# Kernel optimization log

Hardware: AMD Instinct MI355X
Metric: run time of the kernel (lower is better)

The kernel has to match this reference:

```python
import jax, jax.numpy as jnp
import numpy as np

B, DIN, N = 8, 256, 2048  # batch, input_dim (orig node_num), attention nodes (orig seq_len)


def setup_inputs() -> dict:
    key = jax.random.key(0)
    k1, k2, k3, k4 = jax.random.split(key, 4)
    x = jax.random.normal(k1, (B, DIN, N), jnp.float32)
    adj = jax.random.randint(k2, (N, N), 0, 2).astype(jnp.int32)  # binary adjacency
    W = jax.random.normal(k3, (DIN, DIN), jnp.float32) * 0.05      # Linear(D, D, bias=False), stored (out, in)
    a = jax.random.normal(k4, (3 * DIN,), jnp.float32) * 0.05      # Linear(3D, 1, bias=False)
    return {"x": x, "adj": adj, "W": W, "a": a}


def reference(x, adj, W, a):
    # x: (B, D, N) -> permute to (B, N, D); attention is over the N axis
    xt = jnp.transpose(x, (0, 2, 1))
    h = xt @ W.T                                   # (B, N, D)
    sim = jnp.einsum('bid,bjd->bij', h, h)         # (B, N, N) pairwise dot products
    n = adj.shape[0]
    # neighbor mask: adj nonzero, diagonal forced off (mask[:, i] = 0 in the loop)
    m = (adj != 0) & (~jnp.eye(n, dtype=bool))
    # context: the torch loop's weighted_h is independent of its k axis, so
    # context[b, k, i, d] == C[b, i, d] = sum_j m[i,j] * sim[b,i,j] * h[b,j,d]
    C = jnp.einsum('bij,bjd->bid', jnp.where(m[None, :, :], sim, 0.0), h)  # (B, N, D)
    d = h.shape[-1]
    a1, a2, a3 = a[:d], a[d:2 * d], a[2 * d:]
    # a([h_i, h_j, C_j]) = a1.h_i + a2.h_j + a3.C_j  (concat never materialized)
    s_i = h @ a1                                   # (B, N)
    s_j = h @ a2 + C @ a3                          # (B, N)
    scores = jax.nn.leaky_relu(s_i[:, :, None] + s_j[:, None, :], negative_slope=0.2)
    scores = jnp.where(adj[None, :, :] == 0, jnp.float32(-9e15), scores)
    return jax.nn.softmax(scores, axis=-1)         # (B, N, N)
```

## Files before the change

kernel.cpp:

```cpp
#include <hip/hip_runtime.h>
#include <hip/hip_bf16.h>
#include <math.h>

#define Bq   8
#define DINq 256
#define Nq   2048

typedef __attribute__((ext_vector_type(8))) short bf16x8v;
typedef __attribute__((ext_vector_type(4))) float f32x4v;

__device__ __forceinline__ unsigned short f2bf(float f) {
  union { float f; unsigned u; } v; v.f = f;
  unsigned r = v.u + 0x7fffu + ((v.u >> 16) & 1u);
  return (unsigned short)(r >> 16);
}
__device__ __forceinline__ float bf2f(unsigned short h) {
  union { unsigned u; float f; } v; v.u = ((unsigned)h) << 16;
  return v.f;
}

__device__ __forceinline__ void gld_lds16(const void* g, void* l) {
  __builtin_amdgcn_global_load_lds(
      (const __attribute__((address_space(1))) unsigned int*)g,
      (__attribute__((address_space(3))) unsigned int*)l, 16, 0, 0);
}

__global__ void k_prep(const float* __restrict__ W, const float* __restrict__ a,
                       float* __restrict__ w123) {
  int k = threadIdx.x;
  float s1 = 0.f, s2 = 0.f, s3 = 0.f;
  for (int d = 0; d < DINq; ++d) {
    float w = W[d * DINq + k];
    s1 += w * a[d];
    s2 += w * a[DINq + d];
    s3 += w * a[2 * DINq + d];
  }
  w123[k] = s1; w123[DINq + k] = s2; w123[2 * DINq + k] = s3;
}

__global__ void k_transposeW(const float* __restrict__ W, float* __restrict__ WT) {
  int d = blockIdx.x, k = threadIdx.x;
  WT[(size_t)k * DINq + d] = W[(size_t)d * DINq + k];
}

__global__ void k_tsisb(const float* __restrict__ x, const float* __restrict__ w123,
                        float* __restrict__ tA, float* __restrict__ siA,
                        float* __restrict__ sbA) {
  int b = blockIdx.y;
  int il = threadIdx.x & 63;
  int i = blockIdx.x * 64 + il;
  int ks = (threadIdx.x >> 6) * 64;
  float a1 = 0.f, a2 = 0.f, a3 = 0.f;
  for (int k = ks; k < ks + 64; ++k) {
    float xv = x[((size_t)b * DINq + k) * Nq + i];
    a1 += xv * w123[k];
    a2 += xv * w123[DINq + k];
    a3 += xv * w123[2 * DINq + k];
  }
  __shared__ float r1[256], r2[256], r3[256];
  r1[threadIdx.x] = a1; r2[threadIdx.x] = a2; r3[threadIdx.x] = a3;
  __syncthreads();
  if (threadIdx.x < 64) {
    int l = threadIdx.x;
    float v1 = r1[l] + r1[64 + l] + r1[128 + l] + r1[192 + l];
    float v2 = r2[l] + r2[64 + l] + r2[128 + l] + r2[192 + l];
    float v3 = r3[l] + r3[64 + l] + r3[128 + l] + r3[192 + l];
    int ii = blockIdx.x * 64 + l;
    siA[(size_t)b * Nq + ii] = v1;
    sbA[(size_t)b * Nq + ii] = v2;
    tA[(size_t)b * Nq + ii] = v3;
  }
}

__global__ void k_hX(const float* __restrict__ x, const float* __restrict__ WT,
                     const float* __restrict__ tA, float* __restrict__ h,
                     unsigned short* __restrict__ Xhi, unsigned short* __restrict__ Xlo) {
  __shared__ float xs[64][64];
  __shared__ float ws[64][128];
  const int tid = threadIdx.x;
  const int iq = tid & 15;
  const int dg = tid >> 4;
  const int i0 = blockIdx.x * 64;
  const int dh = blockIdx.y;
  const int b = blockIdx.z;

  float acc[4][8];
#pragma unroll
  for (int aa = 0; aa < 4; ++aa)
#pragma unroll
    for (int cc = 0; cc < 8; ++cc) acc[aa][cc] = 0.f;

  for (int kc = 0; kc < 4; ++kc) {
#pragma unroll
    for (int n = 0; n < 16; ++n) {
      int idx = n * 256 + tid;
      int kk = idx >> 6, ii = idx & 63;
      xs[kk][ii] = x[((size_t)b * DINq + kc * 64 + kk) * Nq + i0 + ii];
    }
#pragma unroll
    for (int n = 0; n < 8; ++n) {
      int idx = n * 256 + tid;
      int kk = idx >> 5, c4 = (idx & 31) * 4;
      *(f32x4v*)&ws[kk][c4] =
          *(const f32x4v*)&WT[(size_t)(kc * 64 + kk) * DINq + dh * 128 + c4];
    }
    __syncthreads();
#pragma unroll 4
    for (int kk = 0; kk < 64; ++kk) {
      f32x4v xv = *(const f32x4v*)&xs[kk][iq * 4];
      f32x4v w0 = *(const f32x4v*)&ws[kk][dg * 8];
      f32x4v w1 = *(const f32x4v*)&ws[kk][dg * 8 + 4];
#pragma unroll
      for (int aa = 0; aa < 4; ++aa) {
#pragma unroll
        for (int cc = 0; cc < 4; ++cc) {
          acc[aa][cc]     += xv[aa] * w0[cc];
          acc[aa][cc + 4] += xv[aa] * w1[cc];
        }
      }
    }
    __syncthreads();
  }

  const int ib = i0 + iq * 4;
  float tv[4];
#pragma unroll
  for (int aa = 0; aa < 4; ++aa) tv[aa] = tA[(size_t)b * Nq + ib + aa];

#pragma unroll
  for (int aa = 0; aa < 4; ++aa) {
    size_t hoff = ((size_t)b * Nq + ib + aa) * DINq + dh * 128 + dg * 8;
    f32x4v h0, h1;
#pragma unroll
    for (int cc = 0; cc < 4; ++cc) { h0[cc] = acc[aa][cc]; h1[cc] = acc[aa][cc + 4]; }
    *(f32x4v*)&h[hoff] = h0;
    *(f32x4v*)&h[hoff + 4] = h1;
  }
#pragma unroll
  for (int cc = 0; cc < 8; ++cc) {
    int d = dh * 128 + dg * 8 + cc;
    unsigned short hv[4], lv[4];
#pragma unroll
    for (int aa = 0; aa < 4; ++aa) {
      float Xv = tv[aa] * acc[aa][cc];
      unsigned short hs = f2bf(Xv);
      hv[aa] = hs;
      lv[aa] = f2bf(Xv - bf2f(hs));
    }
    size_t xoff = ((size_t)b * DINq + d) * Nq + ib;
    *(ushort4*)&Xhi[xoff] = make_ushort4(hv[0], hv[1], hv[2], hv[3]);
    *(ushort4*)&Xlo[xoff] = make_ushort4(lv[0], lv[1], lv[2], lv[3]);
  }
}

__global__ void k_mask(const int* __restrict__ adj, unsigned short* __restrict__ Mb) {
  size_t idx = ((size_t)blockIdx.x * 256 + threadIdx.x) * 8;
  int i = (int)(idx >> 11);
  int j0 = (int)(idx & (Nq - 1));
  const int4* ap = (const int4*)&adj[idx];
  int4 a0 = ap[0], a1 = ap[1];
  int av[8] = {a0.x, a0.y, a0.z, a0.w, a1.x, a1.y, a1.z, a1.w};
  unsigned short v[8];
#pragma unroll
  for (int q = 0; q < 8; ++q)
    v[q] = (av[q] != 0 && (j0 + q) != i) ? (unsigned short)0x3F80 : (unsigned short)0;
  ushort4* mp = (ushort4*)&Mb[idx];
  mp[0] = make_ushort4(v[0], v[1], v[2], v[3]);
  mp[1] = make_ushort4(v[4], v[5], v[6], v[7]);
}

__global__ __launch_bounds__(256, 2) void k_gemm(const unsigned short* __restrict__ Mb,
                                                 const unsigned short* __restrict__ Xhi,
                                                 const unsigned short* __restrict__ Xlo,
                                                 const float* __restrict__ h,
                                                 float* __restrict__ sjp) {
  __shared__ __align__(16) unsigned short As[3][128 * 32];
  __shared__ __align__(16) unsigned short Bs[3][128 * 32];
  const int tid = threadIdx.x;
  const int lane = tid & 63;
  const int wave = tid >> 6;
  const int wr = wave >> 1, wc = wave & 1;
  const int i0 = blockIdx.y * 128, c0 = blockIdx.x * 128;
  const int z = blockIdx.z;
  const unsigned short* __restrict__ Xp = z ? Xlo : Xhi;
  const int r15 = lane & 15, kg = lane >> 4;
  const int kb = (kg * 16) ^ ((r15 & 3) << 4);

  f32x4v acc[4][4];
#pragma unroll
  for (int m = 0; m < 4; ++m)
#pragma unroll
    for (int n = 0; n < 4; ++n) acc[m][n] = (f32x4v)0.f;

  auto STAGE = [&](int buf, int t) {
    const int k0 = t * 32;
#pragma unroll
    for (int l = 0; l < 2; ++l) {
      const int c = tid + 256 * l;
      const int row = c >> 2, q = c & 3;
      const int kc = 8 * (q ^ (row & 3));
      gld_lds16(&Mb[(size_t)(i0 + row) * Nq + k0 + kc], &As[buf][c * 8]);
      gld_lds16(&Xp[(size_t)(c0 + row) * Nq + k0 + kc], &Bs[buf][c * 8]);
    }
  };

  constexpr int NT = Nq / 32;
  STAGE(0, 0);
  STAGE(1, 1);
  int cb = 0, sb = 2;
  for (int t = 0; t < NT; ++t) {
    if (t < NT - 2) {
      asm volatile("s_waitcnt vmcnt(4)" ::: "memory");
    } else {
      asm volatile("s_waitcnt vmcnt(0)" ::: "memory");
    }
    __builtin_amdgcn_sched_barrier(0);
    __builtin_amdgcn_s_barrier();
    __builtin_amdgcn_sched_barrier(0);
    if (t + 2 < NT) STAGE(sb, t + 2);

    const char* Ab = (const char*)&As[cb][0];
    const char* Bb = (const char*)&Bs[cb][0];
    bf16x8v af[4], bf[4];
#pragma unroll
    for (int m = 0; m < 4; ++m)
      af[m] = *(const bf16x8v*)(Ab + (wr * 64 + m * 16 + r15) * 64 + kb);
#pragma unroll
    for (int n = 0; n < 4; ++n)
      bf[n] = *(const bf16x8v*)(Bb + (wc * 64 + n * 16 + r15) * 64 + kb);
    __builtin_amdgcn_s_setprio(1);
#pragma unroll
    for (int m = 0; m < 4; ++m)
#pragma unroll
      for (int n = 0; n < 4; ++n)
        acc[m][n] = __builtin_amdgcn_mfma_f32_16x16x32_bf16(af[m], bf[n], acc[m][n], 0, 0, 0);
    __builtin_amdgcn_s_setprio(0);
    cb = (cb == 2) ? 0 : cb + 1;
    sb = (sb == 2) ? 0 : sb + 1;
  }

  const int b = c0 >> 8;
  const int d0 = (c0 & 255) + wc * 64;
  const int re = (lane >> 4) * 4, ce = lane & 15;
  float s[4][4];
#pragma unroll
  for (int m = 0; m < 4; ++m)
#pragma unroll
    for (int r = 0; r < 4; ++r) s[m][r] = 0.f;
#pragma unroll
  for (int m = 0; m < 4; ++m) {
#pragma unroll
    for (int n = 0; n < 4; ++n) {
#pragma unroll
      for (int r = 0; r < 4; ++r) {
        float hv = h[((size_t)b * Nq + i0 + wr * 64 + m * 16 + re + r) * DINq + d0 + n * 16 + ce];
        s[m][r] += acc[m][n][r] * hv;
      }
    }
  }
#pragma unroll
  for (int o = 1; o < 16; o <<= 1) {
#pragma unroll
    for (int m = 0; m < 4; ++m)
#pragma unroll
      for (int r = 0; r < 4; ++r) s[m][r] += __shfl_xor(s[m][r], o, 64);
  }
  if (ce == 0) {
    const int slice = z * 4 + (blockIdx.x & 1) * 2 + wc;
    float* sp = sjp + ((size_t)slice * Bq + b) * Nq;
#pragma unroll
    for (int m = 0; m < 4; ++m)
#pragma unroll
      for (int r = 0; r < 4; ++r)
        sp[i0 + wr * 64 + m * 16 + re + r] = s[m][r];
  }
}

__global__ void k_sjsum(const float* __restrict__ sbA, const float* __restrict__ sjp,
                        float* __restrict__ sjvA) {
  int idx = blockIdx.x * 256 + threadIdx.x;
  float s = sbA[idx];
#pragma unroll
  for (int sl = 0; sl < 8; ++sl) s += sjp[(size_t)sl * Bq * Nq + idx];
  sjvA[idx] = s;
}

__global__ void k_softmax(const int* __restrict__ adj, const float* __restrict__ siA,
                          const float* __restrict__ sjvA, float* __restrict__ out) {
  const int b = blockIdx.y, i = blockIdx.x, tid = threadIdx.x;
  const float siv = siA[(size_t)b * Nq + i];
  const int* arow = adj + (size_t)i * Nq;
  const float* sjb = sjvA + (size_t)b * Nq;
  float sc[8];
  float mx = -3.0e38f;
#pragma unroll
  for (int s = 0; s < 8; ++s) {
    int j = s * 256 + tid;
    float v = siv + sjb[j];
    v = v > 0.f ? v : 0.2f * v;
    v = (arow[j] != 0) ? v : -9.0e15f;
    sc[s] = v;
    mx = fmaxf(mx, v);
  }
#pragma unroll
  for (int o = 32; o >= 1; o >>= 1) mx = fmaxf(mx, __shfl_xor(mx, o, 64));
  __shared__ float redm[4], reds[4];
  const int wave = tid >> 6, lane = tid & 63;
  if (lane == 0) redm[wave] = mx;
  __syncthreads();
  mx = fmaxf(fmaxf(redm[0], redm[1]), fmaxf(redm[2], redm[3]));
  float sum = 0.f, ex[8];
#pragma unroll
  for (int s = 0; s < 8; ++s) { ex[s] = expf(sc[s] - mx); sum += ex[s]; }
#pragma unroll
  for (int o = 32; o >= 1; o >>= 1) sum += __shfl_xor(sum, o, 64);
  if (lane == 0) reds[wave] = sum;
  __syncthreads();
  sum = reds[0] + reds[1] + reds[2] + reds[3];
  float inv = 1.f / sum;
  float* orow = out + ((size_t)b * Nq + i) * Nq;
#pragma unroll
  for (int s = 0; s < 8; ++s) orow[s * 256 + tid] = ex[s] * inv;
}

extern "C" void kernel_launch(void* const* d_in, const int* in_sizes, int n_in,
                              void* d_out, int out_size, void* d_ws, size_t ws_size,
                              hipStream_t stream) {
  const float* x = (const float*)d_in[0];
  const int* adj = (const int*)d_in[1];
  const float* W = (const float*)d_in[2];
  const float* a = (const float*)d_in[3];
  float* out = (float*)d_out;

  char* ws = (char*)d_ws;
  size_t off = 0;
  auto alloc = [&](size_t bytes) -> void* {
    void* p = ws + off;
    off += (bytes + 255) & ~(size_t)255;
    return p;
  };
  float* w123 = (float*)alloc(3 * DINq * sizeof(float));
  float* WT = (float*)alloc((size_t)DINq * DINq * sizeof(float));
  float* tA = (float*)alloc((size_t)Bq * Nq * sizeof(float));
  float* siA = (float*)alloc((size_t)Bq * Nq * sizeof(float));
  float* sbA = (float*)alloc((size_t)Bq * Nq * sizeof(float));
  float* sjvA = (float*)alloc((size_t)Bq * Nq * sizeof(float));
  float* sjp = (float*)alloc((size_t)8 * Bq * Nq * sizeof(float));
  float* h = (float*)alloc((size_t)Bq * Nq * DINq * sizeof(float));
  unsigned short* Xhi = (unsigned short*)alloc((size_t)Nq * Nq * 2);
  unsigned short* Xlo = (unsigned short*)alloc((size_t)Nq * Nq * 2);
  unsigned short* Mb = (unsigned short*)alloc((size_t)Nq * Nq * 2);

  k_prep<<<dim3(1), dim3(256), 0, stream>>>(W, a, w123);
  k_transposeW<<<dim3(DINq), dim3(DINq), 0, stream>>>(W, WT);
  k_tsisb<<<dim3(Nq / 64, Bq), dim3(256), 0, stream>>>(x, w123, tA, siA, sbA);
  k_hX<<<dim3(Nq / 64, 2, Bq), dim3(256), 0, stream>>>(x, WT, tA, h, Xhi, Xlo);
  k_mask<<<dim3(Nq * Nq / (256 * 8)), dim3(256), 0, stream>>>(adj, Mb);
  k_gemm<<<dim3(16, 16, 2), dim3(256), 0, stream>>>(Mb, Xhi, Xlo, h, sjp);
  k_sjsum<<<dim3(Bq * Nq / 256), dim3(256), 0, stream>>>(sbA, sjp, sjvA);
  k_softmax<<<dim3(Nq, Bq), dim3(256), 0, stream>>>(adj, siA, sjvA, out);
}
```

Measured before the change: 150.5 us.

## Fuse score projections into hX, bitpack adjacency, split-K larger GEMM tiles

Removes the separate k_tsisb kernel by computing the si/sb/t projections inside k_hX from the x tiles already in shared memory, which avoids a second full read of x. k_mask now also emits a 1-bit-per-entry adjacency bitmap, so softmax reads 64 words per row instead of 2048 ints. The mask GEMM moves to 256x128 tiles with a two-way split-K and a swizzled 1D grid, doubling the partial slices that k_sjsum reduces. The changes add register pressure in the GEMM (32 accumulators) and extra partial-sum traffic.

New measurement: 151.0 us. No clear change (+0.3%).

```diff
diff --git a/kernel.cpp b/kernel.cpp
--- a/kernel.cpp
+++ b/kernel.cpp
@@ -43,40 +43,15 @@
   WT[(size_t)k * DINq + d] = W[(size_t)d * DINq + k];
 }
 
-__global__ void k_tsisb(const float* __restrict__ x, const float* __restrict__ w123,
-                        float* __restrict__ tA, float* __restrict__ siA,
-                        float* __restrict__ sbA) {
-  int b = blockIdx.y;
-  int il = threadIdx.x & 63;
-  int i = blockIdx.x * 64 + il;
-  int ks = (threadIdx.x >> 6) * 64;
-  float a1 = 0.f, a2 = 0.f, a3 = 0.f;
-  for (int k = ks; k < ks + 64; ++k) {
-    float xv = x[((size_t)b * DINq + k) * Nq + i];
-    a1 += xv * w123[k];
-    a2 += xv * w123[DINq + k];
-    a3 += xv * w123[2 * DINq + k];
-  }
-  __shared__ float r1[256], r2[256], r3[256];
-  r1[threadIdx.x] = a1; r2[threadIdx.x] = a2; r3[threadIdx.x] = a3;
-  __syncthreads();
-  if (threadIdx.x < 64) {
-    int l = threadIdx.x;
-    float v1 = r1[l] + r1[64 + l] + r1[128 + l] + r1[192 + l];
-    float v2 = r2[l] + r2[64 + l] + r2[128 + l] + r2[192 + l];
-    float v3 = r3[l] + r3[64 + l] + r3[128 + l] + r3[192 + l];
-    int ii = blockIdx.x * 64 + l;
-    siA[(size_t)b * Nq + ii] = v1;
-    sbA[(size_t)b * Nq + ii] = v2;
-    tA[(size_t)b * Nq + ii] = v3;
-  }
-}
-
 __global__ void k_hX(const float* __restrict__ x, const float* __restrict__ WT,
-                     const float* __restrict__ tA, float* __restrict__ h,
-                     unsigned short* __restrict__ Xhi, unsigned short* __restrict__ Xlo) {
+                     const float* __restrict__ w123, float* __restrict__ h,
+                     unsigned short* __restrict__ Xhi, unsigned short* __restrict__ Xlo,
+                     float* __restrict__ siA, float* __restrict__ sbA) {
   __shared__ float xs[64][64];
   __shared__ float ws[64][128];
+  __shared__ float wls[3][256];
+  __shared__ float Pd[3][16][64];
+  __shared__ float Tt[64];
   const int tid = threadIdx.x;
   const int iq = tid & 15;
   const int dg = tid >> 4;
@@ -84,11 +59,15 @@
   const int dh = blockIdx.y;
   const int b = blockIdx.z;
 
+  for (int n = tid; n < 768; n += 256) ((float*)wls)[n] = w123[n];
+
   float acc[4][8];
 #pragma unroll
   for (int aa = 0; aa < 4; ++aa)
 #pragma unroll
     for (int cc = 0; cc < 8; ++cc) acc[aa][cc] = 0.f;
+  float p1[4] = {0.f, 0.f, 0.f, 0.f}, p2[4] = {0.f, 0.f, 0.f, 0.f},
+        p3[4] = {0.f, 0.f, 0.f, 0.f};
 
   for (int kc = 0; kc < 4; ++kc) {
 #pragma unroll
@@ -119,13 +98,47 @@
         }
       }
     }
+#pragma unroll
+    for (int kap = 0; kap < 4; ++kap) {
+      int kk = dg * 4 + kap;
+      f32x4v xv = *(const f32x4v*)&xs[kk][iq * 4];
+      float w3 = wls[2][kc * 64 + kk];
+#pragma unroll
+      for (int aa = 0; aa < 4; ++aa) p3[aa] += xv[aa] * w3;
+      if (dh == 0) {
+        float w1 = wls[0][kc * 64 + kk], w2 = wls[1][kc * 64 + kk];
+#pragma unroll
+        for (int aa = 0; aa < 4; ++aa) { p1[aa] += xv[aa] * w1; p2[aa] += xv[aa] * w2; }
+      }
+    }
     __syncthreads();
   }
+
+#pragma unroll
+  for (int aa = 0; aa < 4; ++aa) {
+    Pd[2][dg][iq * 4 + aa] = p3[aa];
+    if (dh == 0) { Pd[0][dg][iq * 4 + aa] = p1[aa]; Pd[1][dg][iq * 4 + aa] = p2[aa]; }
+  }
+  __syncthreads();
+  if (tid < 64) {
+    float t = 0.f, s1 = 0.f, s2 = 0.f;
+#pragma unroll
+    for (int g = 0; g < 16; ++g) {
+      t += Pd[2][g][tid];
+      if (dh == 0) { s1 += Pd[0][g][tid]; s2 += Pd[1][g][tid]; }
+    }
+    Tt[tid] = t;
+    if (dh == 0) {
+      siA[(size_t)b * Nq + i0 + tid] = s1;
+      sbA[(size_t)b * Nq + i0 + tid] = s2;
+    }
+  }
+  __syncthreads();
 
   const int ib = i0 + iq * 4;
   float tv[4];
 #pragma unroll
-  for (int aa = 0; aa < 4; ++aa) tv[aa] = tA[(size_t)b * Nq + ib + aa];
+  for (int aa = 0; aa < 4; ++aa) tv[aa] = Tt[iq * 4 + aa];
 
 #pragma unroll
   for (int aa = 0; aa < 4; ++aa) {
@@ -153,20 +166,30 @@
   }
 }
 
-__global__ void k_mask(const int* __restrict__ adj, unsigned short* __restrict__ Mb) {
-  size_t idx = ((size_t)blockIdx.x * 256 + threadIdx.x) * 8;
-  int i = (int)(idx >> 11);
-  int j0 = (int)(idx & (Nq - 1));
-  const int4* ap = (const int4*)&adj[idx];
-  int4 a0 = ap[0], a1 = ap[1];
-  int av[8] = {a0.x, a0.y, a0.z, a0.w, a1.x, a1.y, a1.z, a1.w};
-  unsigned short v[8];
+__global__ void k_mask(const int* __restrict__ adj, unsigned short* __restrict__ Mb,
+                       unsigned* __restrict__ bm) {
+  int wg = blockIdx.x * 256 + threadIdx.x;
+  int i = wg >> 6, w = wg & 63, j0 = w * 32;
+  const int4* ap = (const int4*)&adj[(size_t)i * Nq + j0];
+  unsigned bits = 0;
+  unsigned short mv[32];
+#pragma unroll
+  for (int q = 0; q < 8; ++q) {
+    int4 a = ap[q];
+    int av[4] = {a.x, a.y, a.z, a.w};
+#pragma unroll
+    for (int e = 0; e < 4; ++e) {
+      int j = j0 + q * 4 + e;
+      bool nz = (av[e] != 0);
+      if (nz) bits |= 1u << (q * 4 + e);
+      mv[q * 4 + e] = (nz && j != i) ? (unsigned short)0x3F80 : (unsigned short)0;
+    }
+  }
+  ushort4* mp = (ushort4*)&Mb[(size_t)i * Nq + j0];
 #pragma unroll
   for (int q = 0; q < 8; ++q)
-    v[q] = (av[q] != 0 && (j0 + q) != i) ? (unsigned short)0x3F80 : (unsigned short)0;
-  ushort4* mp = (ushort4*)&Mb[idx];
-  mp[0] = make_ushort4(v[0], v[1], v[2], v[3]);
-  mp[1] = make_ushort4(v[4], v[5], v[6], v[7]);
+    mp[q] = make_ushort4(mv[q * 4], mv[q * 4 + 1], mv[q * 4 + 2], mv[q * 4 + 3]);
+  bm[wg] = bits;
 }
 
 __global__ __launch_bounds__(256, 2) void k_gemm(const unsigned short* __restrict__ Mb,
@@ -174,86 +197,98 @@
                                                  const unsigned short* __restrict__ Xlo,
                                                  const float* __restrict__ h,
                                                  float* __restrict__ sjp) {
-  __shared__ __align__(16) unsigned short As[3][128 * 32];
+  __shared__ __align__(16) unsigned short As[3][256 * 32];
   __shared__ __align__(16) unsigned short Bs[3][128 * 32];
   const int tid = threadIdx.x;
   const int lane = tid & 63;
   const int wave = tid >> 6;
-  const int wr = wave >> 1, wc = wave & 1;
-  const int i0 = blockIdx.y * 128, c0 = blockIdx.x * 128;
-  const int z = blockIdx.z;
+  const int wm = wave >> 1, wc = wave & 1;
+  const int wg = blockIdx.x;
+  const int lin = (wg & 7) * 64 + (wg >> 3);
+  const int mt = lin >> 6;
+  const int rem = lin & 63;
+  const int ks = rem >> 5;
+  const int z = (rem >> 4) & 1;
+  const int ct = rem & 15;
+  const int i0 = mt * 256, c0 = ct * 128, kbase = ks * 1024;
   const unsigned short* __restrict__ Xp = z ? Xlo : Xhi;
   const int r15 = lane & 15, kg = lane >> 4;
   const int kb = (kg * 16) ^ ((r15 & 3) << 4);
 
-  f32x4v acc[4][4];
-#pragma unroll
-  for (int m = 0; m < 4; ++m)
+  f32x4v acc[8][4];
+#pragma unroll
+  for (int m = 0; m < 8; ++m)
 #pragma unroll
     for (int n = 0; n < 4; ++n) acc[m][n] = (f32x4v)0.f;
 
   auto STAGE = [&](int buf, int t) {
-    const int k0 = t * 32;
+    const int k0 = kbase + t * 32;
+#pragma unroll
+    for (int l = 0; l < 4; ++l) {
+      const int pc = l * 256 + tid;
+      const int row = pc >> 2, q = pc & 3;
+      const int kc = 8 * (q ^ (row & 3));
+      gld_lds16(&Mb[(size_t)(i0 + row) * Nq + k0 + kc], &As[buf][pc * 8]);
+    }
 #pragma unroll
     for (int l = 0; l < 2; ++l) {
-      const int c = tid + 256 * l;
-      const int row = c >> 2, q = c & 3;
+      const int pc = l * 256 + tid;
+      const int row = pc >> 2, q = pc & 3;
       const int kc = 8 * (q ^ (row & 3));
-      gld_lds16(&Mb[(size_t)(i0 + row) * Nq + k0 + kc], &As[buf][c * 8]);
-      gld_lds16(&Xp[(size_t)(c0 + row) * Nq + k0 + kc], &Bs[buf][c * 8]);
+      gld_lds16(&Xp[(size_t)(c0 + row) * Nq + k0 + kc], &Bs[buf][pc * 8]);
     }
   };
 
-  constexpr int NT = Nq / 32;
+  constexpr int NT = 32;
   STAGE(0, 0);
   STAGE(1, 1);
-  int cb = 0, sb = 2;
+  int cb = 0, sb2 = 2;
   for (int t = 0; t < NT; ++t) {
-    if (t < NT - 2) {
-      asm volatile("s_waitcnt vmcnt(4)" ::: "memory");
+    if (t + 1 < NT) {
+      asm volatile("s_waitcnt vmcnt(6)" ::: "memory");
     } else {
       asm volatile("s_waitcnt vmcnt(0)" ::: "memory");
     }
     __builtin_amdgcn_sched_barrier(0);
     __builtin_amdgcn_s_barrier();
     __builtin_amdgcn_sched_barrier(0);
-    if (t + 2 < NT) STAGE(sb, t + 2);
+    if (t + 2 < NT) STAGE(sb2, t + 2);
 
     const char* Ab = (const char*)&As[cb][0];
     const char* Bb = (const char*)&Bs[cb][0];
-    bf16x8v af[4], bf[4];
-#pragma unroll
-    for (int m = 0; m < 4; ++m)
-      af[m] = *(const bf16x8v*)(Ab + (wr * 64 + m * 16 + r15) * 64 + kb);
+    bf16x8v af[8], bf[4];
+#pragma unroll
+    for (int m = 0; m < 8; ++m)
+      af[m] = *(const bf16x8v*)(Ab + (wm * 128 + m * 16 + r15) * 64 + kb);
 #pragma unroll
     for (int n = 0; n < 4; ++n)
       bf[n] = *(const bf16x8v*)(Bb + (wc * 64 + n * 16 + r15) * 64 + kb);
     __builtin_amdgcn_s_setprio(1);
 #pragma unroll
-    for (int m = 0; m < 4; ++m)
+    for (int m = 0; m < 8; ++m)
 #pragma unroll
       for (int n = 0; n < 4; ++n)
         acc[m][n] = __builtin_amdgcn_mfma_f32_16x16x32_bf16(af[m], bf[n], acc[m][n], 0, 0, 0);
     __builtin_amdgcn_s_setprio(0);
     cb = (cb == 2) ? 0 : cb + 1;
-    sb = (sb == 2) ? 0 : sb + 1;
+    sb2 = (sb2 == 2) ? 0 : sb2 + 1;
   }
 
   const int b = c0 >> 8;
   const int d0 = (c0 & 255) + wc * 64;
   const int re = (lane >> 4) * 4, ce = lane & 15;
-  float s[4][4];
-#pragma unroll
-  for (int m = 0; m < 4; ++m)
+  float s[8][4];
+#pragma unroll
+  for (int m = 0; m < 8; ++m)
 #pragma unroll
     for (int r = 0; r < 4; ++r) s[m][r] = 0.f;
 #pragma unroll
-  for (int m = 0; m < 4; ++m) {
+  for (int m = 0; m < 8; ++m) {
 #pragma unroll
     for (int n = 0; n < 4; ++n) {
 #pragma unroll
       for (int r = 0; r < 4; ++r) {
-        float hv = h[((size_t)b * Nq + i0 + wr * 64 + m * 16 + re + r) * DINq + d0 + n * 16 + ce];
+        float hv = h[((size_t)b * Nq + i0 + wm * 128 + m * 16 + re + r) * DINq + d0 + n * 16 + ce];
         s[m][r] += acc[m][n][r] * hv;
       }
     }
@@ -261,18 +296,18 @@
 #pragma unroll
   for (int o = 1; o < 16; o <<= 1) {
 #pragma unroll
-    for (int m = 0; m < 4; ++m)
+    for (int m = 0; m < 8; ++m)
 #pragma unroll
       for (int r = 0; r < 4; ++r) s[m][r] += __shfl_xor(s[m][r], o, 64);
   }
   if (ce == 0) {
-    const int slice = z * 4 + (blockIdx.x & 1) * 2 + wc;
+    const int slice = ks * 8 + z * 4 + (ct & 1) * 2 + wc;
     float* sp = sjp + ((size_t)slice * Bq + b) * Nq;
 #pragma unroll
-    for (int m = 0; m < 4; ++m)
+    for (int m = 0; m < 8; ++m)
 #pragma unroll
       for (int r = 0; r < 4; ++r)
-        sp[i0 + wr * 64 + m * 16 + re + r] = s[m][r];
+        sp[i0 + wm * 128 + m * 16 + re + r] = s[m][r];
   }
 }
 
@@ -281,16 +316,17 @@
   int idx = blockIdx.x * 256 + threadIdx.x;
   float s = sbA[idx];
 #pragma unroll
-  for (int sl = 0; sl < 8; ++sl) s += sjp[(size_t)sl * Bq * Nq + idx];
+  for (int sl = 0; sl < 16; ++sl) s += sjp[(size_t)sl * Bq * Nq + idx];
   sjvA[idx] = s;
 }
 
-__global__ void k_softmax(const int* __restrict__ adj, const float* __restrict__ siA,
+__global__ void k_softmax(const unsigned* __restrict__ bm, const float* __restrict__ siA,
                           const float* __restrict__ sjvA, float* __restrict__ out) {
   const int b = blockIdx.y, i = blockIdx.x, tid = threadIdx.x;
   const float siv = siA[(size_t)b * Nq + i];
-  const int* arow = adj + (size_t)i * Nq;
+  const unsigned* brow = bm + (size_t)i * 64;
   const float* sjb = sjvA + (size_t)b * Nq;
+  const int bit = tid & 31;
   float sc[8];
   float mx = -3.0e38f;
 #pragma unroll
@@ -298,7 +334,8 @@
     int j = s * 256 + tid;
     float v = siv + sjb[j];
     v = v > 0.f ? v : 0.2f * v;
-    v = (arow[j] != 0) ? v : -9.0e15f;
+    unsigned wv = brow[j >> 5];
+    v = ((wv >> bit) & 1u) ? v : -9.0e15f;
     sc[s] = v;
     mx = fmaxf(mx, v);
   }
@@ -341,22 +378,21 @@
   };
   float* w123 = (float*)alloc(3 * DINq * sizeof(float));
   float* WT = (float*)alloc((size_t)DINq * DINq * sizeof(float));
-  float* tA = (float*)alloc((size_t)Bq * Nq * sizeof(float));
   float* siA = (float*)alloc((size_t)Bq * Nq * sizeof(float));
   float* sbA = (float*)alloc((size_t)Bq * Nq * sizeof(float));
   float* sjvA = (float*)alloc((size_t)Bq * Nq * sizeof(float));
-  float* sjp = (float*)alloc((size_t)8 * Bq * Nq * sizeof(float));
+  float* sjp = (float*)alloc((size_t)16 * Bq * Nq * sizeof(float));
   float* h = (float*)alloc((size_t)Bq * Nq * DINq * sizeof(float));
   unsigned short* Xhi = (unsigned short*)alloc((size_t)Nq * Nq * 2);
   unsigned short* Xlo = (unsigned short*)alloc((size_t)Nq * Nq * 2);
   unsigned short* Mb = (unsigned short*)alloc((size_t)Nq * Nq * 2);
+  unsigned* bm = (unsigned*)alloc((size_t)Nq * 64 * sizeof(unsigned));
 
   k_prep<<<dim3(1), dim3(256), 0, stream>>>(W, a, w123);
   k_transposeW<<<dim3(DINq), dim3(DINq), 0, stream>>>(W, WT);
-  k_tsisb<<<dim3(Nq / 64, Bq), dim3(256), 0, stream>>>(x, w123, tA, siA, sbA);
-  k_hX<<<dim3(Nq / 64, 2, Bq), dim3(256), 0, stream>>>(x, WT, tA, h, Xhi, Xlo);
-  k_mask<<<dim3(Nq * Nq / (256 * 8)), dim3(256), 0, stream>>>(adj, Mb);
-  k_gemm<<<dim3(16, 16, 2), dim3(256), 0, stream>>>(Mb, Xhi, Xlo, h, sjp);
+  k_hX<<<dim3(Nq / 64, 2, Bq), dim3(256), 0, stream>>>(x, WT, w123, h, Xhi, Xlo, siA, sbA);
+  k_mask<<<dim3(Nq * 64 / 256), dim3(256), 0, stream>>>(adj, Mb, bm);
+  k_gemm<<<dim3(512), dim3(256), 0, stream>>>(Mb, Xhi, Xlo, h, sjp);
   k_sjsum<<<dim3(Bq * Nq / 256), dim3(256), 0, stream>>>(sbA, sjp, sjvA);
-  k_softmax<<<dim3(Nq, Bq), dim3(256), 0, stream>>>(adj, siA, sjvA, out);
-}
+  k_softmax<<<dim3(Nq, Bq), dim3(256), 0, stream>>>(bm, siA, sjvA, out);
+}
```
